# Kernel tuning notes

Hardware: AMD Instinct MI355X
Metric: run time of the kernel (lower is better)

The kernel has to match this reference:

```python
import math
import jax, jax.numpy as jnp
import numpy as np

B, S, T, C, H = 4, 100, 128, 256, 256
NH, DH = 4, 32            # num_attention_heads//2, hidden_size//num_attention_heads
AH = NH * DH              # all_head_size = 128
FH = 32                   # fire_hidden_size
MAX_SP, MAX_TM, MAX_DOY = 180.0, 365.0, 182.0


def _fire(dist, c, w1, w2, max_dist):
    # FIREDistanceBias: log-compressed distance -> MLP(1->FH, SiLU, FH->1, no bias)
    c = jnp.maximum(c, 0.0)
    d = jnp.log(c * dist + 1.0) / jnp.log(c * max_dist + 1.0)
    h = jax.nn.silu(d[..., None] * w1[:, 0])   # (..., FH)
    return h @ w2[0]                            # (...,)


def setup_inputs() -> dict:
    key = jax.random.key(0)
    ks = jax.random.split(key, 20)
    p = 0.02
    inp = {
        "hidden_states": jax.random.normal(ks[0], (B, S, T, H), jnp.float32),
        "source_embeddings": jax.random.normal(ks[1], (B, S, C, H), jnp.float32),
        "attention_mask": jnp.zeros((B, 1, 1, T, C), jnp.float32),
        "st_dist": jax.random.uniform(ks[2], (B, T, C, 2), jnp.float32)
                   * jnp.array([MAX_SP, MAX_TM], jnp.float32),
        "st_doy_dist": jax.random.uniform(ks[3], (B, T, C), jnp.float32) * MAX_DOY,
        # attention projections (Linear H->AH with bias), output dense (AH->H)
        "Wq": jax.random.normal(ks[4], (AH, H), jnp.float32) * p,
        "bq": jnp.zeros((AH,), jnp.float32),
        "Wk": jax.random.normal(ks[5], (AH, H), jnp.float32) * p,
        "bk": jnp.zeros((AH,), jnp.float32),
        "Wv": jax.random.normal(ks[6], (AH, H), jnp.float32) * p,
        "bv": jnp.zeros((AH,), jnp.float32),
        "Wo": jax.random.normal(ks[7], (H, AH), jnp.float32) * p,
        "bo": jnp.zeros((H,), jnp.float32),
        # FIRE params: spatial / temporal / seasonal
        "c_s": jnp.float32(100.0),
        "w1_s": jax.random.normal(ks[8], (FH, 1), jnp.float32) * 0.5,
        "w2_s": jax.random.normal(ks[9], (1, FH), jnp.float32) * 0.5,
        "c_t": jnp.float32(100.0),
        "w1_t": jax.random.normal(ks[10], (FH, 1), jnp.float32) * 0.5,
        "w2_t": jax.random.normal(ks[11], (1, FH), jnp.float32) * 0.5,
        "c_d": jnp.float32(100.0),
        "w1_d": jax.random.normal(ks[12], (FH, 1), jnp.float32) * 0.5,
        "w2_d": jax.random.normal(ks[13], (1, FH), jnp.float32) * 0.5,
        # per-species log scales (init zeros in torch)
        "s_log_scale": jnp.zeros((S,), jnp.float32),
        "t_log_scale": jnp.zeros((S,), jnp.float32),
    }
    return inp


def reference(hidden_states, source_embeddings, attention_mask, st_dist, st_doy_dist,
              Wq, bq, Wk, bk, Wv, bv, Wo, bo,
              c_s, w1_s, w2_s, c_t, w1_t, w2_t, c_d, w1_d, w2_d,
              s_log_scale, t_log_scale):
    # FIRE distance biases over (B, T, C)
    sb = _fire(st_dist[..., 0], c_s, w1_s, w2_s, MAX_SP)
    tb = _fire(st_dist[..., 1], c_t, w1_t, w2_t, MAX_TM)
    db = _fire(st_doy_dist, c_d, w1_d, w2_d, MAX_DOY)
    # (B, S, T, C): species-scaled spatial+temporal + seasonal bias
    bias = (sb[:, None] * jnp.exp(s_log_scale)[None, :, None, None]
            + tb[:, None] * jnp.exp(t_log_scale)[None, :, None, None]
            + db[:, None])

    # projections; split heads: (B,S,L,AH) -> (B,S,NH,L,DH)
    q = (hidden_states @ Wq.T + bq).reshape(B, S, T, NH, DH).transpose(0, 1, 3, 2, 4)
    k = (source_embeddings @ Wk.T + bk).reshape(B, S, C, NH, DH).transpose(0, 1, 3, 2, 4)
    v = (source_embeddings @ Wv.T + bv).reshape(B, S, C, NH, DH).transpose(0, 1, 3, 2, 4)

    scores = jnp.einsum('bshtd,bshcd->bshtc', q, k) / math.sqrt(DH)
    scores = scores + attention_mask + bias[:, :, None]   # mask (B,1,1,T,C), bias (B,S,1,T,C)
    probs = jax.nn.softmax(scores, axis=-1)
    ctx = jnp.einsum('bshtc,bshcd->bshtd', probs, v)
    ctx = ctx.transpose(0, 1, 3, 2, 4).reshape(B, S, T, AH)
    return ctx @ Wo.T + bo   # STCrossOutput dense (dropout=0, eval)
```

## Files before the change

kernel.cpp:

```cpp
#include <hip/hip_runtime.h>
#include <hip/hip_bf16.h>
#include <math.h>

#define Bdim 4
#define Sdim 100
#define Tdim 128
#define Cdim 256
#define Hdim 256
#define NHd  4
#define DHd  32
#define AHd  128

typedef short bf16x8 __attribute__((ext_vector_type(8)));
typedef float f32x4 __attribute__((ext_vector_type(4)));

#define WAITCNT_V(n) do { \
  asm volatile("s_waitcnt vmcnt(" #n ")" ::: "memory"); \
  __builtin_amdgcn_sched_barrier(0); \
} while (0)

__device__ __forceinline__ short f2b(float x) {
  unsigned u = __float_as_uint(x);
  unsigned r = (u + 0x7FFF + ((u >> 16) & 1)) >> 16;
  return (short)r;
}

__device__ __forceinline__ void split2(float x, short& hi, short& lo) {
  unsigned u = __float_as_uint(x) & 0xFFFF0000u;
  hi = (short)(u >> 16);
  lo = f2b(x - __uint_as_float(u));
}

__device__ __forceinline__ float fire_eval(float dist, float c,
                                           const float* __restrict__ w1,
                                           const float* __restrict__ w2,
                                           float maxd) {
  c = fmaxf(c, 0.0f);
  float d = logf(fmaf(c, dist, 1.0f)) / logf(fmaf(c, maxd, 1.0f));
  float acc = 0.0f;
#pragma unroll
  for (int j = 0; j < 32; ++j) {
    float x = d * w1[j];
    float h = x / (1.0f + expf(-x));
    acc = fmaf(h, w2[j], acc);
  }
  return acc;
}

__global__ __launch_bounds__(256) void fire_bias_kernel(
    const float* __restrict__ st_dist, const float* __restrict__ st_doy,
    const float* __restrict__ mask,
    const float* __restrict__ c_s, const float* __restrict__ w1_s, const float* __restrict__ w2_s,
    const float* __restrict__ c_t, const float* __restrict__ w1_t, const float* __restrict__ w2_t,
    const float* __restrict__ c_d, const float* __restrict__ w1_d, const float* __restrict__ w2_d,
    float4* __restrict__ pk) {
  int i = blockIdx.x * 256 + threadIdx.x;
  if (i >= Bdim * Tdim * Cdim) return;
  float2 dv = ((const float2*)st_dist)[i];
  float4 r;
  r.x = fire_eval(dv.x, c_s[0], w1_s, w2_s, 180.0f);
  r.y = fire_eval(dv.y, c_t[0], w1_t, w2_t, 365.0f);
  r.z = fire_eval(st_doy[i], c_d[0], w1_d, w2_d, 182.0f) + mask[i];
  r.w = 0.0f;
  pk[i] = r;
}

__global__ __launch_bounds__(256) void wsplit_pack(
    const float* __restrict__ Wq, const float* __restrict__ Wk,
    const float* __restrict__ Wv, const float* __restrict__ Wo,
    short* __restrict__ pack) {
  int which = blockIdx.y;
  const float* W = which == 0 ? Wq : which == 1 ? Wk : which == 2 ? Wv : Wo;
  int idx = blockIdx.x * 256 + threadIdx.x;
  int j = idx & 7;
  int l = (idx >> 3) & 63;
  int frag = idx >> 9;
  int nt, kk8, Kd;
  if (which == 3) { nt = frag & 15; kk8 = frag >> 4; Kd = 128; }
  else           { nt = frag & 7;  kk8 = frag >> 3; Kd = 256; }
  int n = nt * 16 + (l & 15);
  int k = kk8 * 32 + (l >> 4) * 8 + j;
  float val = W[(size_t)n * Kd + k];
  short h, lo_;
  if (which == 3) split2(val, h, lo_);
  else { h = f2b(val); lo_ = 0; }
  pack[(size_t)which * 65536 + idx] = h;
  pack[(size_t)which * 65536 + 32768 + idx] = lo_;
}

__global__ __launch_bounds__(256, 2) void phase1(
    const float* __restrict__ se,
    const short* __restrict__ Wkp, const float* __restrict__ bk,
    const short* __restrict__ Wvp, const float* __restrict__ bv,
    short* __restrict__ Ko, short* __restrict__ Vo,
    const float* __restrict__ hs, const short* __restrict__ Wqp,
    const float* __restrict__ bq, short* __restrict__ Qb, float scale,
    const float4* __restrict__ pk,
    const float* __restrict__ sls, const float* __restrict__ tls,
    float* __restrict__ bF) {
  __shared__ short wlds[2][16 * 512];
  const int bid = blockIdx.x;
  const int tid = threadIdx.x;
  const int l = tid & 63, w = tid >> 6;
  const int lr = l & 15, lg = l >> 4;

  if (bid < 800) {
    const int m0 = bid * 128;
    const float* ap0 = se + (size_t)(m0 + w * 32 + lr) * 256 + lg * 8;
    const float* ap1 = ap0 + (size_t)16 * 256;

    auto stage = [&](int buf, int kk) {
#pragma unroll
      for (int r = 0; r < 4; ++r) {
        int f = w + 4 * r;
        const short* gsrc = ((f >> 3) ? Wvp : Wkp) + ((size_t)(kk * 8 + (f & 7)) * 64 + l) * 8;
        int loff = __builtin_amdgcn_readfirstlane(buf * 8192 + f * 512);
        __builtin_amdgcn_global_load_lds(gsrc, &wlds[0][0] + loff, 16, 0, 0);
      }
    };

    f32x4 accK[2][8] = {}, accV[2][8] = {};
    stage(0, 0);
    float4 c0a = *(const float4*)ap0;
    float4 c0b = *(const float4*)(ap0 + 4);
    float4 c1a = *(const float4*)ap1;
    float4 c1b = *(const float4*)(ap1 + 4);
#pragma unroll
    for (int kk = 0; kk < 8; ++kk) {
      const int buf = kk & 1;
      float4 n0a, n0b, n1a, n1b;
      if (kk < 7) {
        stage(buf ^ 1, kk + 1);
        const int nk = (kk + 1) * 32;
        n0a = *(const float4*)(ap0 + nk);
        n0b = *(const float4*)(ap0 + nk + 4);
        n1a = *(const float4*)(ap1 + nk);
        n1b = *(const float4*)(ap1 + nk + 4);
      }
      bf16x8 af[2];
      {
        float a0[8] = {c0a.x, c0a.y, c0a.z, c0a.w, c0b.x, c0b.y, c0b.z, c0b.w};
        float a1[8] = {c1a.x, c1a.y, c1a.z, c1a.w, c1b.x, c1b.y, c1b.z, c1b.w};
#pragma unroll
        for (int e = 0; e < 8; ++e) { af[0][e] = f2b(a0[e]); af[1][e] = f2b(a1[e]); }
      }
      if (kk < 7) { WAITCNT_V(8); } else { WAITCNT_V(0); }
      __builtin_amdgcn_s_barrier();
      const short* lb = &wlds[0][0] + buf * 8192 + l * 8;
#pragma unroll
      for (int nt = 0; nt < 8; ++nt) {
        bf16x8 kw = *(const bf16x8*)(lb + nt * 512);
        bf16x8 vw = *(const bf16x8*)(lb + (8 + nt) * 512);
#pragma unroll
        for (int mi = 0; mi < 2; ++mi) {
          accK[mi][nt] = __builtin_amdgcn_mfma_f32_16x16x32_bf16(af[mi], kw, accK[mi][nt], 0, 0, 0);
          accV[mi][nt] = __builtin_amdgcn_mfma_f32_16x16x32_bf16(af[mi], vw, accV[mi][nt], 0, 0, 0);
        }
      }
      __builtin_amdgcn_s_barrier();
      if (kk < 7) { c0a = n0a; c0b = n0b; c1a = n1a; c1b = n1b; }
    }
#pragma unroll
    for (int mi = 0; mi < 2; ++mi)
#pragma unroll
      for (int nt = 0; nt < 8; ++nt)
#pragma unroll
        for (int r = 0; r < 4; ++r) {
          size_t row = (size_t)(m0 + w * 32 + mi * 16 + lg * 4 + r) * 128 + nt * 16 + lr;
          Ko[row] = f2b(accK[mi][nt][r] + bk[nt * 16 + lr]);
          Vo[row] = f2b(accV[mi][nt][r] + bv[nt * 16 + lr]);
        }
  } else if (bid < 1200) {
    const int m0 = (bid - 800) * 128;
    const float* ap0 = hs + (size_t)(m0 + w * 32 + lr) * 256 + lg * 8;
    const float* ap1 = ap0 + (size_t)16 * 256;

    auto stage = [&](int buf, int kk) {
#pragma unroll
      for (int r = 0; r < 2; ++r) {
        int f = w + 4 * r;
        const short* gsrc = Wqp + ((size_t)(kk * 8 + f) * 64 + l) * 8;
        int loff = __builtin_amdgcn_readfirstlane(buf * 8192 + f * 512);
        __builtin_amdgcn_global_load_lds(gsrc, &wlds[0][0] + loff, 16, 0, 0);
      }
    };

    f32x4 acc[2][8] = {};
    stage(0, 0);
    float4 c0a = *(const float4*)ap0;
    float4 c0b = *(const float4*)(ap0 + 4);
    float4 c1a = *(const float4*)ap1;
    float4 c1b = *(const float4*)(ap1 + 4);
#pragma unroll
    for (int kk = 0; kk < 8; ++kk) {
      const int buf = kk & 1;
      float4 n0a, n0b, n1a, n1b;
      if (kk < 7) {
        stage(buf ^ 1, kk + 1);
        const int nk = (kk + 1) * 32;
        n0a = *(const float4*)(ap0 + nk);
        n0b = *(const float4*)(ap0 + nk + 4);
        n1a = *(const float4*)(ap1 + nk);
        n1b = *(const float4*)(ap1 + nk + 4);
      }
      bf16x8 af[2];
      {
        float a0[8] = {c0a.x, c0a.y, c0a.z, c0a.w, c0b.x, c0b.y, c0b.z, c0b.w};
        float a1[8] = {c1a.x, c1a.y, c1a.z, c1a.w, c1b.x, c1b.y, c1b.z, c1b.w};
#pragma unroll
        for (int e = 0; e < 8; ++e) { af[0][e] = f2b(a0[e]); af[1][e] = f2b(a1[e]); }
      }
      if (kk < 7) { WAITCNT_V(6); } else { WAITCNT_V(0); }
      __builtin_amdgcn_s_barrier();
      const short* lb = &wlds[0][0] + buf * 8192 + l * 8;
#pragma unroll
      for (int nt = 0; nt < 8; ++nt) {
        bf16x8 wv = *(const bf16x8*)(lb + nt * 512);
#pragma unroll
        for (int mi = 0; mi < 2; ++mi)
          acc[mi][nt] = __builtin_amdgcn_mfma_f32_16x16x32_bf16(af[mi], wv, acc[mi][nt], 0, 0, 0);
      }
      __builtin_amdgcn_s_barrier();
      if (kk < 7) { c0a = n0a; c0b = n0b; c1a = n1a; c1b = n1b; }
    }
#pragma unroll
    for (int mi = 0; mi < 2; ++mi)
#pragma unroll
      for (int nt = 0; nt < 8; ++nt)
#pragma unroll
        for (int r = 0; r < 4; ++r)
          Qb[(size_t)(m0 + w * 32 + mi * 16 + lg * 4 + r) * 128 + nt * 16 + lr] =
              f2b((acc[mi][nt][r] + bq[nt * 16 + lr]) * scale);
  } else {
    const int bb_ = bid - 1200;
    const int nt = (bb_ & 3) * 4 + w;
    const int wt = (bb_ >> 2) & 7;
    const int b  = bb_ >> 5;
    const int c = nt * 16 + lr;
    float sb[4], tb[4], db[4];
#pragma unroll
    for (int r = 0; r < 4; ++r) {
      float4 v = pk[(size_t)b * Tdim * Cdim + (size_t)(wt * 16 + lg * 4 + r) * Cdim + c];
      sb[r] = v.x; tb[r] = v.y; db[r] = v.z;
    }
    for (int s = 0; s < Sdim; ++s) {
      float es = __expf(sls[s]), et = __expf(tls[s]);
      float4 o;
      o.x = fmaf(sb[0], es, fmaf(tb[0], et, db[0]));
      o.y = fmaf(sb[1], es, fmaf(tb[1], et, db[1]));
      o.z = fmaf(sb[2], es, fmaf(tb[2], et, db[2]));
      o.w = fmaf(sb[3], es, fmaf(tb[3], et, db[3]));
      size_t idx = ((((size_t)(b * Sdim + s) * 8 + wt) * 16 + nt) * 64 + l);
      *(float4*)(bF + idx * 4) = o;
    }
  }
}

__global__ __launch_bounds__(256, 2) void proj_o_mfma(
    const short* __restrict__ Ahi, const short* __restrict__ Alo,
    const short* __restrict__ Wp, const float* __restrict__ bias,
    float* __restrict__ O) {
  __shared__ short wlds[2][32 * 512];
  const int tid = threadIdx.x;
  const int l = tid & 63, w = tid >> 6;
  const int lr = l & 15, lg = l >> 4;
  const int m0 = blockIdx.x * 128;
  const short* ah0 = Ahi + (size_t)(m0 + w * 32 + lr) * 128 + lg * 8;
  const short* al0 = Alo + (size_t)(m0 + w * 32 + lr) * 128 + lg * 8;
  const short* ah1 = ah0 + (size_t)16 * 128;
  const short* al1 = al0 + (size_t)16 * 128;

  auto stage = [&](int buf, int kk) {
#pragma unroll
    for (int r = 0; r < 8; ++r) {
      int f = w + 4 * r;
      const short* gsrc = Wp + ((f >> 4) ? 32768 : 0)
                          + ((size_t)(kk * 16 + (f & 15)) * 64 + l) * 8;
      int loff = __builtin_amdgcn_readfirstlane(buf * 16384 + f * 512);
      __builtin_amdgcn_global_load_lds(gsrc, &wlds[0][0] + loff, 16, 0, 0);
    }
  };

  f32x4 acc[2][16] = {};
  stage(0, 0);
  bf16x8 ch0 = *(const bf16x8*)ah0;
  bf16x8 cl0 = *(const bf16x8*)al0;
  bf16x8 ch1 = *(const bf16x8*)ah1;
  bf16x8 cl1 = *(const bf16x8*)al1;
#pragma unroll
  for (int kk = 0; kk < 4; ++kk) {
    const int buf = kk & 1;
    bf16x8 nh0, nl0, nh1, nl1;
    if (kk < 3) {
      stage(buf ^ 1, kk + 1);
      const int nk = (kk + 1) * 32;
      nh0 = *(const bf16x8*)(ah0 + nk);
      nl0 = *(const bf16x8*)(al0 + nk);
      nh1 = *(const bf16x8*)(ah1 + nk);
      nl1 = *(const bf16x8*)(al1 + nk);
    }
    if (kk < 3) { WAITCNT_V(12); } else { WAITCNT_V(0); }
    __builtin_amdgcn_s_barrier();
    bf16x8 ahi[2] = {ch0, ch1};
    bf16x8 alo[2] = {cl0, cl1};
    const short* lb = &wlds[0][0] + buf * 16384 + l * 8;
#pragma unroll
    for (int nt = 0; nt < 16; ++nt) {
      bf16x8 whi = *(const bf16x8*)(lb + nt * 512);
      bf16x8 wlo = *(const bf16x8*)(lb + (16 + nt) * 512);
#pragma unroll
      for (int mi = 0; mi < 2; ++mi) {
        acc[mi][nt] = __builtin_amdgcn_mfma_f32_16x16x32_bf16(ahi[mi], whi, acc[mi][nt], 0, 0, 0);
        acc[mi][nt] = __builtin_amdgcn_mfma_f32_16x16x32_bf16(ahi[mi], wlo, acc[mi][nt], 0, 0, 0);
        acc[mi][nt] = __builtin_amdgcn_mfma_f32_16x16x32_bf16(alo[mi], whi, acc[mi][nt], 0, 0, 0);
      }
    }
    __builtin_amdgcn_s_barrier();
    if (kk < 3) { ch0 = nh0; cl0 = nl0; ch1 = nh1; cl1 = nl1; }
  }
#pragma unroll
  for (int mi = 0; mi < 2; ++mi)
#pragma unroll
    for (int nt = 0; nt < 16; ++nt)
#pragma unroll
      for (int r = 0; r < 4; ++r)
        O[(size_t)(m0 + w * 32 + mi * 16 + lg * 4 + r) * 256 + nt * 16 + lr] =
            acc[mi][nt][r] + bias[nt * 16 + lr];
}

__global__ __launch_bounds__(512, 2) void attn_mfma(
    const short* __restrict__ Qb, const short* __restrict__ Kb,
    const short* __restrict__ Vb,
    const float* __restrict__ bF,
    short* __restrict__ Chi, short* __restrict__ Clo) {
  __shared__ short vfrag[8][2][64][8];
  __shared__ short pbuf[8][16 * 36];

  const int tid = threadIdx.x;
  const int l = tid & 63;
  const int w = tid >> 6;
  const int lr = l & 15, lg = l >> 4;
  const int bid = blockIdx.x;
  const int xcd = bid & 7;
  const int i_  = bid >> 3;
  const int bs  = xcd * 50 + (i_ >> 2);
  const int h   = i_ & 3;

  const size_t kvbase = (size_t)bs * Cdim * AHd + h * DHd;
  const size_t qbase  = (size_t)bs * Tdim * AHd + h * DHd;

  bf16x8 qf = *(const bf16x8*)(Qb + qbase + (size_t)(w * 16 + lr) * AHd + lg * 8);
  bf16x8 kf[16];
#pragma unroll
  for (int nt = 0; nt < 16; ++nt)
    kf[nt] = *(const bf16x8*)(Kb + kvbase + (size_t)(nt * 16 + lr) * AHd + lg * 8);

#pragma unroll
  for (int rep = 0; rep < 2; ++rep) {
    int chunk = tid * 2 + rep;
    int c = chunk >> 2, q = chunk & 3;
    bf16x8 v8 = *(const bf16x8*)(Vb + kvbase + (size_t)c * AHd + q * 8);
    int kc = c >> 5, nt = q >> 1;
    int lanebase = ((c & 31) >> 3) * 16 + (q & 1) * 8;
    int j = c & 7;
#pragma unroll
    for (int e = 0; e < 8; ++e) {
      int row = lanebase + e;
      int prow = row ^ ((row >> 4) << 1);
      vfrag[kc][nt][prow][j] = v8[e];
    }
  }
  __syncthreads();

  const float4* bb = (const float4*)bF + ((size_t)bs * 8 + w) * 16 * 64 + l;
  f32x4 sacc[16];
#pragma unroll
  for (int nt = 0; nt < 16; ++nt) {
    float4 cv = bb[nt * 64];
    f32x4 cinit = {cv.x, cv.y, cv.z, cv.w};
    sacc[nt] = __builtin_amdgcn_mfma_f32_16x16x32_bf16(qf, kf[nt], cinit, 0, 0, 0);
  }

  float rinv[4];
#pragma unroll
  for (int nt = 0; nt < 16; ++nt)
#pragma unroll
    for (int r = 0; r < 4; ++r)
      sacc[nt][r] = __expf(sacc[nt][r]);
#pragma unroll
  for (int r = 0; r < 4; ++r) {
    float su = 0.f;
#pragma unroll
    for (int nt = 0; nt < 16; ++nt) su += sacc[nt][r];
#pragma unroll
    for (int off = 1; off < 16; off <<= 1) su += __shfl_xor(su, off);
    rinv[r] = 1.0f / su;
  }

  const f32x4 zero = {0.f, 0.f, 0.f, 0.f};
  f32x4 cacc[2] = {zero, zero};
  short* pb = &pbuf[w][0];
  const int lp = l ^ ((l >> 4) << 1);
#pragma unroll
  for (int kc = 0; kc < 8; ++kc) {
#pragma unroll
    for (int ntl = 0; ntl < 2; ++ntl) {
      int nt = kc * 2 + ntl;
#pragma unroll
      for (int r = 0; r < 4; ++r)
        pb[(lg * 4 + r) * 36 + ntl * 16 + lr] = f2b(sacc[nt][r]);
    }
    bf16x8 af = *(const bf16x8*)&pb[lr * 36 + lg * 8];
#pragma unroll
    for (int ntd = 0; ntd < 2; ++ntd) {
      bf16x8 vf = *(const bf16x8*)&vfrag[kc][ntd][lp][0];
      cacc[ntd] = __builtin_amdgcn_mfma_f32_16x16x32_bf16(af, vf, cacc[ntd], 0, 0, 0);
    }
  }

#pragma unroll
  for (int ntd = 0; ntd < 2; ++ntd)
#pragma unroll
    for (int r = 0; r < 4; ++r) {
      float val = cacc[ntd][r] * rinv[r];
      short h_, lo_;
      split2(val, h_, lo_);
      size_t idx = qbase + (size_t)(w * 16 + lg * 4 + r) * AHd + ntd * 16 + lr;
      Chi[idx] = h_;
      Clo[idx] = lo_;
    }
}

extern "C" void kernel_launch(void* const* d_in, const int* in_sizes, int n_in,
                              void* d_out, int out_size, void* d_ws, size_t ws_size,
                              hipStream_t stream) {
  const float* hs     = (const float*)d_in[0];
  const float* se     = (const float*)d_in[1];
  const float* mask   = (const float*)d_in[2];
  const float* stdist = (const float*)d_in[3];
  const float* stdoy  = (const float*)d_in[4];
  const float* Wq = (const float*)d_in[5];
  const float* bq = (const float*)d_in[6];
  const float* Wk = (const float*)d_in[7];
  const float* bk = (const float*)d_in[8];
  const float* Wv = (const float*)d_in[9];
  const float* bv = (const float*)d_in[10];
  const float* Wo = (const float*)d_in[11];
  const float* bo = (const float*)d_in[12];
  const float* c_s  = (const float*)d_in[13];
  const float* w1_s = (const float*)d_in[14];
  const float* w2_s = (const float*)d_in[15];
  const float* c_t  = (const float*)d_in[16];
  const float* w1_t = (const float*)d_in[17];
  const float* w2_t = (const float*)d_in[18];
  const float* c_d  = (const float*)d_in[19];
  const float* w1_d = (const float*)d_in[20];
  const float* w2_d = (const float*)d_in[21];
  const float* sls  = (const float*)d_in[22];
  const float* tls  = (const float*)d_in[23];
  float* out = (float*)d_out;

  float* ws = (float*)d_ws;
  const size_t BTC  = (size_t)Bdim * Tdim * Cdim;
  const size_t BSTC = (size_t)Bdim * Sdim * Tdim * Cdim;
  const size_t NQ   = (size_t)Bdim * Sdim * Tdim * AHd;
  const size_t NKV  = (size_t)Bdim * Sdim * Cdim * AHd;

  float4* pk  = (float4*)ws;
  float* bF   = ws + 4 * BTC;
  short* wpck = (short*)(bF + BSTC);
  short* Qb   = wpck + 262144;
  short* Kb   = Qb + NQ;
  short* Vb   = Kb + NKV;
  short* Chi  = Vb + NKV;
  short* Clo  = Chi + NQ;

  const int MQ  = Bdim * Sdim * Tdim;

  fire_bias_kernel<<<(Bdim * Tdim * Cdim + 255) / 256, 256, 0, stream>>>(
      stdist, stdoy, mask, c_s, w1_s, w2_s, c_t, w1_t, w2_t, c_d, w1_d, w2_d, pk);

  wsplit_pack<<<dim3(128, 4), 256, 0, stream>>>(Wq, Wk, Wv, Wo, wpck);

  phase1<<<dim3(1328), 256, 0, stream>>>(
      se, wpck + 65536, bk, wpck + 131072, bv, Kb, Vb,
      hs, wpck, bq, Qb, 0.17677669529663687f,
      pk, sls, tls, bF);

  attn_mfma<<<dim3(Bdim * Sdim * NHd), 512, 0, stream>>>(
      Qb, Kb, Vb, bF, Chi, Clo);

  proj_o_mfma<<<dim3(MQ / 128), 256, 0, stream>>>(Chi, Clo, wpck + 196608, bo, out);
}
```

Before: 156.0 us.

## Compute per-species bias inside attention instead of materializing full bias tensor

Drops the phase1 branch that wrote a full (B,S,T,C) fp32 bias tensor. The FIRE kernel now writes three small (B,T,C) arrays already in MFMA fragment layout, and the attention kernel combines them with exp(s_log_scale) and exp(t_log_scale) per species on the fly. This removes about 52MB of writes and re-reads in exchange for three smaller loads and a few FMAs per score fragment. Phase1 blocks are also interleaved K/V, K/V, Q so the block mix is more uniform across the grid.

```diff
diff --git a/kernel.cpp b/kernel.cpp
--- a/kernel.cpp
+++ b/kernel.cpp
@@ -53,16 +53,22 @@
     const float* __restrict__ c_s, const float* __restrict__ w1_s, const float* __restrict__ w2_s,
     const float* __restrict__ c_t, const float* __restrict__ w1_t, const float* __restrict__ w2_t,
     const float* __restrict__ c_d, const float* __restrict__ w1_d, const float* __restrict__ w2_d,
-    float4* __restrict__ pk) {
+    float* __restrict__ sbF, float* __restrict__ tbF, float* __restrict__ dbF) {
   int i = blockIdx.x * 256 + threadIdx.x;
   if (i >= Bdim * Tdim * Cdim) return;
+  int c = i & (Cdim - 1);
+  int t = (i >> 8) & (Tdim - 1);
+  int b = i >> 15;
   float2 dv = ((const float2*)st_dist)[i];
-  float4 r;
-  r.x = fire_eval(dv.x, c_s[0], w1_s, w2_s, 180.0f);
-  r.y = fire_eval(dv.y, c_t[0], w1_t, w2_t, 365.0f);
-  r.z = fire_eval(st_doy[i], c_d[0], w1_d, w2_d, 182.0f) + mask[i];
-  r.w = 0.0f;
-  pk[i] = r;
+  float sv = fire_eval(dv.x, c_s[0], w1_s, w2_s, 180.0f);
+  float tv = fire_eval(dv.y, c_t[0], w1_t, w2_t, 365.0f);
+  float db = fire_eval(st_doy[i], c_d[0], w1_d, w2_d, 182.0f) + mask[i];
+  int wt = t >> 4, lg = (t & 15) >> 2, r = t & 3;
+  int nt = c >> 4, lr = c & 15;
+  size_t off = ((((size_t)(b * 8 + wt) * 16 + nt) * 64) + lg * 16 + lr) * 4 + r;
+  sbF[off] = sv;
+  tbF[off] = tv;
+  dbF[off] = db;
 }
 
 __global__ __launch_bounds__(256) void wsplit_pack(
@@ -94,18 +100,16 @@
     const short* __restrict__ Wvp, const float* __restrict__ bv,
     short* __restrict__ Ko, short* __restrict__ Vo,
     const float* __restrict__ hs, const short* __restrict__ Wqp,
-    const float* __restrict__ bq, short* __restrict__ Qb, float scale,
-    const float4* __restrict__ pk,
-    const float* __restrict__ sls, const float* __restrict__ tls,
-    float* __restrict__ bF) {
+    const float* __restrict__ bq, short* __restrict__ Qb, float scale) {
   __shared__ short wlds[2][16 * 512];
   const int bid = blockIdx.x;
   const int tid = threadIdx.x;
   const int l = tid & 63, w = tid >> 6;
   const int lr = l & 15, lg = l >> 4;
-
-  if (bid < 800) {
-    const int m0 = bid * 128;
+  const int g = bid / 3, m = bid - g * 3;
+
+  if (m < 2) {
+    const int m0 = (g * 2 + m) * 128;
     const float* ap0 = se + (size_t)(m0 + w * 32 + lr) * 256 + lg * 8;
     const float* ap1 = ap0 + (size_t)16 * 256;
 
@@ -170,8 +174,8 @@
           Ko[row] = f2b(accK[mi][nt][r] + bk[nt * 16 + lr]);
           Vo[row] = f2b(accV[mi][nt][r] + bv[nt * 16 + lr]);
         }
-  } else if (bid < 1200) {
-    const int m0 = (bid - 800) * 128;
+  } else {
+    const int m0 = g * 128;
     const float* ap0 = hs + (size_t)(m0 + w * 32 + lr) * 256 + lg * 8;
     const float* ap1 = ap0 + (size_t)16 * 256;
 
@@ -231,28 +235,6 @@
         for (int r = 0; r < 4; ++r)
           Qb[(size_t)(m0 + w * 32 + mi * 16 + lg * 4 + r) * 128 + nt * 16 + lr] =
               f2b((acc[mi][nt][r] + bq[nt * 16 + lr]) * scale);
-  } else {
-    const int bb_ = bid - 1200;
-    const int nt = (bb_ & 3) * 4 + w;
-    const int wt = (bb_ >> 2) & 7;
-    const int b  = bb_ >> 5;
-    const int c = nt * 16 + lr;
-    float sb[4], tb[4], db[4];
-#pragma unroll
-    for (int r = 0; r < 4; ++r) {
-      float4 v = pk[(size_t)b * Tdim * Cdim + (size_t)(wt * 16 + lg * 4 + r) * Cdim + c];
-      sb[r] = v.x; tb[r] = v.y; db[r] = v.z;
-    }
-    for (int s = 0; s < Sdim; ++s) {
-      float es = __expf(sls[s]), et = __expf(tls[s]);
-      float4 o;
-      o.x = fmaf(sb[0], es, fmaf(tb[0], et, db[0]));
-      o.y = fmaf(sb[1], es, fmaf(tb[1], et, db[1]));
-      o.z = fmaf(sb[2], es, fmaf(tb[2], et, db[2]));
-      o.w = fmaf(sb[3], es, fmaf(tb[3], et, db[3]));
-      size_t idx = ((((size_t)(b * Sdim + s) * 8 + wt) * 16 + nt) * 64 + l);
-      *(float4*)(bF + idx * 4) = o;
-    }
   }
 }
 
@@ -331,7 +313,9 @@
 __global__ __launch_bounds__(512, 2) void attn_mfma(
     const short* __restrict__ Qb, const short* __restrict__ Kb,
     const short* __restrict__ Vb,
-    const float* __restrict__ bF,
+    const float* __restrict__ sbF, const float* __restrict__ tbF,
+    const float* __restrict__ dbF,
+    const float* __restrict__ sls, const float* __restrict__ tls,
     short* __restrict__ Chi, short* __restrict__ Clo) {
   __shared__ short vfrag[8][2][64][8];
   __shared__ short pbuf[8][16 * 36];
@@ -345,6 +329,9 @@
   const int i_  = bid >> 3;
   const int bs  = xcd * 50 + (i_ >> 2);
   const int h   = i_ & 3;
+  const int s = bs % Sdim, b = bs / Sdim;
+  const float es = __expf(sls[s]);
+  const float et = __expf(tls[s]);
 
   const size_t kvbase = (size_t)bs * Cdim * AHd + h * DHd;
   const size_t qbase  = (size_t)bs * Tdim * AHd + h * DHd;
@@ -372,12 +359,21 @@
   }
   __syncthreads();
 
-  const float4* bb = (const float4*)bF + ((size_t)bs * 8 + w) * 16 * 64 + l;
+  const size_t bfrag = ((size_t)(b * 8 + w) * 16) * 64 + l;
+  const float4* sb4 = (const float4*)sbF + bfrag;
+  const float4* tb4 = (const float4*)tbF + bfrag;
+  const float4* db4 = (const float4*)dbF + bfrag;
   f32x4 sacc[16];
 #pragma unroll
   for (int nt = 0; nt < 16; ++nt) {
-    float4 cv = bb[nt * 64];
-    f32x4 cinit = {cv.x, cv.y, cv.z, cv.w};
+    float4 sv = sb4[nt * 64];
+    float4 tv = tb4[nt * 64];
+    float4 dv = db4[nt * 64];
+    f32x4 cinit;
+    cinit[0] = fmaf(sv.x, es, fmaf(tv.x, et, dv.x));
+    cinit[1] = fmaf(sv.y, es, fmaf(tv.y, et, dv.y));
+    cinit[2] = fmaf(sv.z, es, fmaf(tv.z, et, dv.z));
+    cinit[3] = fmaf(sv.w, es, fmaf(tv.w, et, dv.w));
     sacc[nt] = __builtin_amdgcn_mfma_f32_16x16x32_bf16(qf, kf[nt], cinit, 0, 0, 0);
   }
 
@@ -462,13 +458,13 @@
 
   float* ws = (float*)d_ws;
   const size_t BTC  = (size_t)Bdim * Tdim * Cdim;
-  const size_t BSTC = (size_t)Bdim * Sdim * Tdim * Cdim;
   const size_t NQ   = (size_t)Bdim * Sdim * Tdim * AHd;
   const size_t NKV  = (size_t)Bdim * Sdim * Cdim * AHd;
 
-  float4* pk  = (float4*)ws;
-  float* bF   = ws + 4 * BTC;
-  short* wpck = (short*)(bF + BSTC);
+  float* sbF  = ws;
+  float* tbF  = sbF + BTC;
+  float* dbF  = tbF + BTC;
+  short* wpck = (short*)(dbF + BTC);
   short* Qb   = wpck + 262144;
   short* Kb   = Qb + NQ;
   short* Vb   = Kb + NKV;
@@ -478,17 +474,17 @@
   const int MQ  = Bdim * Sdim * Tdim;
 
   fire_bias_kernel<<<(Bdim * Tdim * Cdim + 255) / 256, 256, 0, stream>>>(
-      stdist, stdoy, mask, c_s, w1_s, w2_s, c_t, w1_t, w2_t, c_d, w1_d, w2_d, pk);
+      stdist, stdoy, mask, c_s, w1_s, w2_s, c_t, w1_t, w2_t, c_d, w1_d, w2_d,
+      sbF, tbF, dbF);
 
   wsplit_pack<<<dim3(128, 4), 256, 0, stream>>>(Wq, Wk, Wv, Wo, wpck);
 
-  phase1<<<dim3(1328), 256, 0, stream>>>(
+  phase1<<<dim3(1200), 256, 0, stream>>>(
       se, wpck + 65536, bk, wpck + 131072, bv, Kb, Vb,
-      hs, wpck, bq, Qb, 0.17677669529663687f,
-      pk, sls, tls, bF);
+      hs, wpck, bq, Qb, 0.17677669529663687f);
 
   attn_mfma<<<dim3(Bdim * Sdim * NHd), 512, 0, stream>>>(
-      Qb, Kb, Vb, bF, Chi, Clo);
+      Qb, Kb, Vb, sbF, tbF, dbF, sls, tls, Chi, Clo);
 
   proj_o_mfma<<<dim3(MQ / 128), 256, 0, stream>>>(Chi, Clo, wpck + 196608, bo, out);
 }
```

After: 164.5 us. 1.05x slower.
